# Optimization experiments

Hardware: AMD Instinct MI355X
Metric: run time of the kernel (lower is better)

Reference implementation:

```python
import jax, jax.numpy as jnp
import numpy as np


def setup_inputs() -> dict:
    key = jax.random.key(0)
    ks = jax.random.split(key, 8)
    B, N, H = 8, 64, 256
    nE, E = 256, 64
    HID, OUT = 512, 1
    s1 = 1.0 / np.sqrt(H + E)
    s2 = 1.0 / np.sqrt(HID)
    return {
        "h_all": jax.random.normal(ks[0], (B, N, H), dtype=jnp.float32),
        "e_feat": jax.random.normal(ks[1], (nE, E), dtype=jnp.float32),
        "W1": jax.random.normal(ks[2], (H + E, HID), dtype=jnp.float32) * s1,
        "b1": jnp.zeros((HID,), dtype=jnp.float32),
        "W2": jax.random.normal(ks[3], (HID, HID), dtype=jnp.float32) * s2,
        "b2": jnp.zeros((HID,), dtype=jnp.float32),
        "W3": jax.random.normal(ks[4], (HID, OUT), dtype=jnp.float32) * s2,
        "b3": jnp.zeros((OUT,), dtype=jnp.float32),
    }


def reference(h_all, e_feat, W1, b1, W2, b2, W3, b3):
    # Math == MLP(cat([expand(h), expand(e)], -1)) but computed via split
    # weights: cat([h,e]) @ W1 == h @ W1[:H] + e @ W1[H:], avoiding the
    # materialized [B,N,nE,H+E] concat tensor.
    H = h_all.shape[-1]
    Wh, We = W1[:H], W1[H:]
    h_part = jnp.einsum("bnh,hk->bnk", h_all, Wh)        # [B,N,HID]
    e_part = jnp.einsum("ed,dk->ek", e_feat, We)          # [nE,HID]
    x = h_part[:, :, None, :] + e_part[None, None, :, :] + b1  # [B,N,nE,HID]
    x = jax.nn.relu(x)
    x = jax.nn.relu(jnp.einsum("bnek,kj->bnej", x, W2) + b2)
    return jnp.einsum("bnek,ko->bneo", x, W3) + b3        # [B,N,nE,OUT]
```

## Files before the change

### kernel.cpp

```cpp
#include <hip/hip_runtime.h>
#include <hip/hip_bf16.h>


typedef __attribute__((ext_vector_type(8))) short bf16x8;
typedef __attribute__((ext_vector_type(4))) float f32x4;

static __device__ __forceinline__ ushort2 pk_bf16(float a, float b) {
  union { __hip_bfloat162 h; ushort2 u; } c;
  c.h = __float22bfloat162_rn(make_float2(a, b));
  return c.u;
}
static __device__ __forceinline__ float bf2f(unsigned short u) {
  union { unsigned int i; float f; } c;
  c.i = ((unsigned int)u) << 16;
  return c.f;
}

__global__ __launch_bounds__(256) void k_prep(
    const float* __restrict__ h_all, const float* __restrict__ e_feat,
    const float* __restrict__ W1, const float* __restrict__ b1,
    const float* __restrict__ W2,
    unsigned short* __restrict__ hpb, unsigned short* __restrict__ epb,
    unsigned short* __restrict__ w2f) {
  __shared__ float sm[64 * 68];
  const int t = threadIdx.x;
  const int b = blockIdx.x;

  if (b < 256) {
    const int r0 = b * 2;
    float (*hs)[256] = (float(*)[256])sm;
    hs[0][t] = h_all[(size_t)r0 * 256 + t];
    hs[1][t] = h_all[(size_t)(r0 + 1) * 256 + t];
    __syncthreads();
    float2 a0 = make_float2(0.f, 0.f), a1 = make_float2(0.f, 0.f);
    #pragma unroll 2
    for (int k = 0; k < 256; k += 4) {
      float2 w0 = *(const float2*)(W1 + (size_t)k * 512 + 2 * t);
      float2 w1 = *(const float2*)(W1 + (size_t)(k + 1) * 512 + 2 * t);
      float2 w2v = *(const float2*)(W1 + (size_t)(k + 2) * 512 + 2 * t);
      float2 w3v = *(const float2*)(W1 + (size_t)(k + 3) * 512 + 2 * t);
      float h00 = hs[0][k], h01 = hs[0][k + 1], h02 = hs[0][k + 2], h03 = hs[0][k + 3];
      float h10 = hs[1][k], h11 = hs[1][k + 1], h12 = hs[1][k + 2], h13 = hs[1][k + 3];
      a0.x = fmaf(h00, w0.x, a0.x); a0.y = fmaf(h00, w0.y, a0.y);
      a1.x = fmaf(h10, w0.x, a1.x); a1.y = fmaf(h10, w0.y, a1.y);
      a0.x = fmaf(h01, w1.x, a0.x); a0.y = fmaf(h01, w1.y, a0.y);
      a1.x = fmaf(h11, w1.x, a1.x); a1.y = fmaf(h11, w1.y, a1.y);
      a0.x = fmaf(h02, w2v.x, a0.x); a0.y = fmaf(h02, w2v.y, a0.y);
      a1.x = fmaf(h12, w2v.x, a1.x); a1.y = fmaf(h12, w2v.y, a1.y);
      a0.x = fmaf(h03, w3v.x, a0.x); a0.y = fmaf(h03, w3v.y, a0.y);
      a1.x = fmaf(h13, w3v.x, a1.x); a1.y = fmaf(h13, w3v.y, a1.y);
    }
    float2 bv = *(const float2*)(b1 + 2 * t);
    *(ushort2*)(hpb + (size_t)r0 * 512 + 2 * t) = pk_bf16(a0.x + bv.x, a0.y + bv.y);
    *(ushort2*)(hpb + (size_t)(r0 + 1) * 512 + 2 * t) = pk_bf16(a1.x + bv.x, a1.y + bv.y);
  } else if (b < 288) {
    const int r0 = (b - 256) * 8;
    sm[t] = e_feat[(size_t)r0 * 64 + t];
    sm[256 + t] = e_feat[(size_t)r0 * 64 + 256 + t];
    __syncthreads();
    float2 acc[8];
    #pragma unroll
    for (int i = 0; i < 8; ++i) acc[i] = make_float2(0.f, 0.f);
    for (int k = 0; k < 64; ++k) {
      float2 wv = *(const float2*)(W1 + (size_t)(256 + k) * 512 + 2 * t);
      #pragma unroll
      for (int i = 0; i < 8; ++i) {
        acc[i].x = fmaf(sm[i * 64 + k], wv.x, acc[i].x);
        acc[i].y = fmaf(sm[i * 64 + k], wv.y, acc[i].y);
      }
    }
    #pragma unroll
    for (int i = 0; i < 8; ++i)
      *(ushort2*)(epb + (size_t)(r0 + i) * 512 + 2 * t) = pk_bf16(acc[i].x, acc[i].y);
  } else {
    const int bb = b - 288;
    const int k0 = (bb >> 3) * 64;
    const int c0 = (bb & 7) * 64;
    #pragma unroll
    for (int rr = 0; rr < 4; ++rr) {
      const int row = rr * 16 + (t >> 4);
      float4 v = *(const float4*)(W2 + (size_t)(k0 + row) * 512 + c0 + (t & 15) * 4);
      *(float4*)(&sm[row * 68 + (t & 15) * 4]) = v;
    }
    __syncthreads();
    #pragma unroll
    for (int s2 = 0; s2 < 2; ++s2) {
      const int s = t * 2 + s2;
      const int rec = s >> 6, l = s & 63;
      const int jg = (c0 >> 4) + (rec & 3);
      const int ksg = (k0 >> 5) + (rec >> 2);
      const int cl = (rec & 3) * 16 + (l & 15);
      const int kl = (rec >> 2) * 32 + (l >> 4) * 8;
      union { ushort2 o[4]; uint4 v; } u;
      #pragma unroll
      for (int uu = 0; uu < 4; ++uu)
        u.o[uu] = pk_bf16(sm[(kl + 2 * uu) * 68 + cl], sm[(kl + 2 * uu + 1) * 68 + cl]);
      *(uint4*)(w2f + ((size_t)(jg * 16 + ksg) * 64 + l) * 8) = u.v;
    }
  }
}

__global__ __launch_bounds__(256, 2) void k_main(
    const unsigned short* __restrict__ hpb, const unsigned short* __restrict__ epb,
    const unsigned short* __restrict__ w2f, const float* __restrict__ b2,
    const float* __restrict__ W3, const float* __restrict__ b3,
    float* __restrict__ out) {
  __shared__ unsigned short x1s[64 * 512];

  const int t = threadIdx.x;
  const int lane = t & 63;
  const int w = t >> 6;
  const int l15 = lane & 15, l4 = lane >> 4;
  const int bn = blockIdx.x >> 2;
  const int e0 = (blockIdx.x & 3) << 6;
  const int off = (blockIdx.x * 11) & 15;
  const unsigned short* hprow = hpb + (size_t)bn * 512;

  const unsigned short* wrec = w2f + (size_t)w * 65536 + (size_t)lane * 8;
  bf16x8 bb[2][8];
  #pragma unroll
  for (int j = 0; j < 8; ++j) {
    bb[0][j] = *(const bf16x8*)(wrec + j * 8192 + (size_t)off * 512);
    bb[1][j] = *(const bf16x8*)(wrec + j * 8192 + (size_t)((off + 1) & 15) * 512);
  }

  {
    const int kk = t & 63;
    const int rbase = t >> 6;
    union { uint4 v; unsigned short s[8]; } hv, ev, ov;
    hv.v = *(const uint4*)(hprow + kk * 8);
    float hf[8];
    #pragma unroll
    for (int u = 0; u < 8; ++u) hf[u] = bf2f(hv.s[u]);
    #pragma unroll 2
    for (int rr = 0; rr < 16; ++rr) {
      const int r = rr * 4 + rbase;
      ev.v = *(const uint4*)(epb + (size_t)(e0 + r) * 512 + kk * 8);
      #pragma unroll
      for (int u = 0; u < 4; ++u) {
        ushort2 p = pk_bf16(fmaxf(bf2f(ev.s[2 * u]) + hf[2 * u], 0.f),
                            fmaxf(bf2f(ev.s[2 * u + 1]) + hf[2 * u + 1], 0.f));
        ov.s[2 * u] = p.x;
        ov.s[2 * u + 1] = p.y;
      }
      *(uint4*)(&x1s[r * 512 + (kk ^ (r & 7)) * 8]) = ov.v;
    }
  }
  __syncthreads();

  f32x4 acc[4][8] = {};
  #pragma unroll 4
  for (int ks = 0; ks < 16; ++ks) {
    const int cur = ks & 1;
    const int kr = (ks + off) & 15;
    const int kr2 = (ks + 2 + off) & 15;
    bf16x8 a[4];
    #pragma unroll
    for (int i = 0; i < 4; ++i) {
      const int r = i * 16 + l15;
      a[i] = *(const bf16x8*)(&x1s[r * 512 + (((kr * 4 + l4) ^ (l15 & 7)) * 8)]);
    }
    #pragma unroll
    for (int i = 0; i < 4; ++i)
      #pragma unroll
      for (int j = 0; j < 8; ++j)
        acc[i][j] = __builtin_amdgcn_mfma_f32_16x16x32_bf16(a[i], bb[cur][j], acc[i][j], 0, 0, 0);
    #pragma unroll
    for (int j = 0; j < 8; ++j)
      bb[cur][j] = *(const bf16x8*)(wrec + j * 8192 + (size_t)kr2 * 512);
  }

  float part[16];
  #pragma unroll
  for (int u = 0; u < 16; ++u) part[u] = 0.f;
  #pragma unroll
  for (int j = 0; j < 8; ++j) {
    const int n = w * 128 + j * 16 + l15;
    const float b2v = b2[n], w3v = W3[n];
    #pragma unroll
    for (int i = 0; i < 4; ++i)
      #pragma unroll
      for (int r = 0; r < 4; ++r)
        part[i * 4 + r] = fmaf(fmaxf(acc[i][j][r] + b2v, 0.f), w3v, part[i * 4 + r]);
  }
  #pragma unroll
  for (int u = 0; u < 16; ++u) {
    float v = part[u];
    v += __shfl_xor(v, 1);
    v += __shfl_xor(v, 2);
    v += __shfl_xor(v, 4);
    v += __shfl_xor(v, 8);
    part[u] = v;
  }
  __syncthreads();
  float* osum = (float*)x1s;
  if (l15 == 0) {
    #pragma unroll
    for (int i = 0; i < 4; ++i)
      #pragma unroll
      for (int r = 0; r < 4; ++r)
        osum[w * 64 + i * 16 + l4 * 4 + r] = part[i * 4 + r];
  }
  __syncthreads();
  if (t < 64) {
    float s = b3[0] + osum[t] + osum[64 + t] + osum[128 + t] + osum[192 + t];
    out[(size_t)bn * 256 + e0 + t] = s;
  }
}

extern "C" void kernel_launch(void* const* d_in, const int* in_sizes, int n_in,
                              void* d_out, int out_size, void* d_ws, size_t ws_size,
                              hipStream_t stream) {
  const float* h_all  = (const float*)d_in[0];
  const float* e_feat = (const float*)d_in[1];
  const float* W1     = (const float*)d_in[2];
  const float* b1     = (const float*)d_in[3];
  const float* W2     = (const float*)d_in[4];
  const float* b2     = (const float*)d_in[5];
  const float* W3     = (const float*)d_in[6];
  const float* b3     = (const float*)d_in[7];
  float* out = (float*)d_out;

  unsigned short* hpb = (unsigned short*)d_ws;
  unsigned short* epb = hpb + 512 * 512;
  unsigned short* w2f = epb + 256 * 512;

  hipLaunchKernelGGL(k_prep, dim3(352), dim3(256), 0, stream,
                     h_all, e_feat, W1, b1, W2, hpb, epb, w2f);
  hipLaunchKernelGGL(k_main, dim3(2048), dim3(256), 0, stream,
                     hpb, epb, w2f, b2, W3, b3, out);
}
```

Measured before the change: 145.3 us.

## Switch main GEMM to 32x32x16 MFMA with 512-thread blocks and 8 waves

Replaces the 16x16x32 bf16 MFMA tiling (4 waves each computing 64x128) with 32x32x16 MFMA over 8 waves each computing 64x64. The W2 fragment layout written by the prep kernel is changed to match. Block size goes to 512 threads with launch bounds for higher occupancy, and the epilogue reduction is adapted to 32-lane groups and 8 partial sums. The aim is fewer B-register fragments per wave and better MFMA efficiency. The cost is twice as many waves sharing the LDS tile and a larger epilogue reduction.

```diff
diff --git a/kernel.cpp b/kernel.cpp
--- a/kernel.cpp
+++ b/kernel.cpp
@@ -3,7 +3,7 @@
 
 
 typedef __attribute__((ext_vector_type(8))) short bf16x8;
-typedef __attribute__((ext_vector_type(4))) float f32x4;
+typedef __attribute__((ext_vector_type(16))) float f32x16;
 
 static __device__ __forceinline__ ushort2 pk_bf16(float a, float b) {
   union { __hip_bfloat162 h; ushort2 u; } c;
@@ -73,9 +73,9 @@
     for (int i = 0; i < 8; ++i)
       *(ushort2*)(epb + (size_t)(r0 + i) * 512 + 2 * t) = pk_bf16(acc[i].x, acc[i].y);
   } else {
-    const int bb = b - 288;
-    const int k0 = (bb >> 3) * 64;
-    const int c0 = (bb & 7) * 64;
+    const int bbk = b - 288;
+    const int k0 = (bbk >> 3) * 64;
+    const int c0 = (bbk & 7) * 64;
     #pragma unroll
     for (int rr = 0; rr < 4; ++rr) {
       const int row = rr * 16 + (t >> 4);
@@ -87,20 +87,20 @@
     for (int s2 = 0; s2 < 2; ++s2) {
       const int s = t * 2 + s2;
       const int rec = s >> 6, l = s & 63;
-      const int jg = (c0 >> 4) + (rec & 3);
-      const int ksg = (k0 >> 5) + (rec >> 2);
-      const int cl = (rec & 3) * 16 + (l & 15);
-      const int kl = (rec >> 2) * 32 + (l >> 4) * 8;
+      const int jg = (c0 >> 5) + (rec & 1);
+      const int ks = (k0 >> 4) + (rec >> 1);
+      const int cl = (rec & 1) * 32 + (l & 31);
+      const int kl = (rec >> 1) * 16 + (l >> 5) * 8;
       union { ushort2 o[4]; uint4 v; } u;
       #pragma unroll
       for (int uu = 0; uu < 4; ++uu)
         u.o[uu] = pk_bf16(sm[(kl + 2 * uu) * 68 + cl], sm[(kl + 2 * uu + 1) * 68 + cl]);
-      *(uint4*)(w2f + ((size_t)(jg * 16 + ksg) * 64 + l) * 8) = u.v;
-    }
-  }
-}
-
-__global__ __launch_bounds__(256, 2) void k_main(
+      *(uint4*)(w2f + ((size_t)(jg * 32 + ks) * 64 + l) * 8) = u.v;
+    }
+  }
+}
+
+__global__ __launch_bounds__(512, 4) void k_main(
     const unsigned short* __restrict__ hpb, const unsigned short* __restrict__ epb,
     const unsigned short* __restrict__ w2f, const float* __restrict__ b2,
     const float* __restrict__ W3, const float* __restrict__ b3,
@@ -110,19 +110,19 @@
   const int t = threadIdx.x;
   const int lane = t & 63;
   const int w = t >> 6;
-  const int l15 = lane & 15, l4 = lane >> 4;
+  const int l31 = lane & 31, l5 = lane >> 5;
   const int bn = blockIdx.x >> 2;
   const int e0 = (blockIdx.x & 3) << 6;
-  const int off = (blockIdx.x * 11) & 15;
+  const int off = (blockIdx.x * 7) & 31;
   const unsigned short* hprow = hpb + (size_t)bn * 512;
 
-  const unsigned short* wrec = w2f + (size_t)w * 65536 + (size_t)lane * 8;
-  bf16x8 bb[2][8];
-  #pragma unroll
-  for (int j = 0; j < 8; ++j) {
-    bb[0][j] = *(const bf16x8*)(wrec + j * 8192 + (size_t)off * 512);
-    bb[1][j] = *(const bf16x8*)(wrec + j * 8192 + (size_t)((off + 1) & 15) * 512);
-  }
+  const unsigned short* wrec0 = w2f + (size_t)(w * 2) * 16384 + (size_t)lane * 8;
+  const unsigned short* wrec1 = wrec0 + 16384;
+  bf16x8 bb[2][2];
+  bb[0][0] = *(const bf16x8*)(wrec0 + (size_t)off * 512);
+  bb[0][1] = *(const bf16x8*)(wrec1 + (size_t)off * 512);
+  bb[1][0] = *(const bf16x8*)(wrec0 + (size_t)((off + 1) & 31) * 512);
+  bb[1][1] = *(const bf16x8*)(wrec1 + (size_t)((off + 1) & 31) * 512);
 
   {
     const int kk = t & 63;
@@ -132,9 +132,9 @@
     float hf[8];
     #pragma unroll
     for (int u = 0; u < 8; ++u) hf[u] = bf2f(hv.s[u]);
-    #pragma unroll 2
-    for (int rr = 0; rr < 16; ++rr) {
-      const int r = rr * 4 + rbase;
+    #pragma unroll 4
+    for (int rr = 0; rr < 8; ++rr) {
+      const int r = rr * 8 + rbase;
       ev.v = *(const uint4*)(epb + (size_t)(e0 + r) * 512 + kk * 8);
       #pragma unroll
       for (int u = 0; u < 4; ++u) {
@@ -148,62 +148,65 @@
   }
   __syncthreads();
 
-  f32x4 acc[4][8] = {};
+  const int xr = l31 & 7;
+  f32x16 acc[2][2] = {};
   #pragma unroll 4
-  for (int ks = 0; ks < 16; ++ks) {
+  for (int ks = 0; ks < 32; ++ks) {
     const int cur = ks & 1;
-    const int kr = (ks + off) & 15;
-    const int kr2 = (ks + 2 + off) & 15;
-    bf16x8 a[4];
-    #pragma unroll
-    for (int i = 0; i < 4; ++i) {
-      const int r = i * 16 + l15;
-      a[i] = *(const bf16x8*)(&x1s[r * 512 + (((kr * 4 + l4) ^ (l15 & 7)) * 8)]);
-    }
-    #pragma unroll
-    for (int i = 0; i < 4; ++i)
-      #pragma unroll
-      for (int j = 0; j < 8; ++j)
-        acc[i][j] = __builtin_amdgcn_mfma_f32_16x16x32_bf16(a[i], bb[cur][j], acc[i][j], 0, 0, 0);
-    #pragma unroll
-    for (int j = 0; j < 8; ++j)
-      bb[cur][j] = *(const bf16x8*)(wrec + j * 8192 + (size_t)kr2 * 512);
-  }
-
-  float part[16];
+    const int kr = (ks + off) & 31;
+    const int kr2 = (ks + 2 + off) & 31;
+    const int c0 = ((kr * 2 + l5) ^ xr) * 8;
+    bf16x8 a0 = *(const bf16x8*)(&x1s[l31 * 512 + c0]);
+    bf16x8 a1 = *(const bf16x8*)(&x1s[(l31 + 32) * 512 + c0]);
+    acc[0][0] = __builtin_amdgcn_mfma_f32_32x32x16_bf16(a0, bb[cur][0], acc[0][0], 0, 0, 0);
+    acc[1][0] = __builtin_amdgcn_mfma_f32_32x32x16_bf16(a1, bb[cur][0], acc[1][0], 0, 0, 0);
+    acc[0][1] = __builtin_amdgcn_mfma_f32_32x32x16_bf16(a0, bb[cur][1], acc[0][1], 0, 0, 0);
+    acc[1][1] = __builtin_amdgcn_mfma_f32_32x32x16_bf16(a1, bb[cur][1], acc[1][1], 0, 0, 0);
+    bb[cur][0] = *(const bf16x8*)(wrec0 + (size_t)kr2 * 512);
+    bb[cur][1] = *(const bf16x8*)(wrec1 + (size_t)kr2 * 512);
+  }
+
+  float part[2][16];
   #pragma unroll
-  for (int u = 0; u < 16; ++u) part[u] = 0.f;
+  for (int rt = 0; rt < 2; ++rt)
+    #pragma unroll
+    for (int r = 0; r < 16; ++r) part[rt][r] = 0.f;
   #pragma unroll
-  for (int j = 0; j < 8; ++j) {
-    const int n = w * 128 + j * 16 + l15;
+  for (int ct = 0; ct < 2; ++ct) {
+    const int n = w * 64 + ct * 32 + l31;
     const float b2v = b2[n], w3v = W3[n];
     #pragma unroll
-    for (int i = 0; i < 4; ++i)
-      #pragma unroll
-      for (int r = 0; r < 4; ++r)
-        part[i * 4 + r] = fmaf(fmaxf(acc[i][j][r] + b2v, 0.f), w3v, part[i * 4 + r]);
+    for (int rt = 0; rt < 2; ++rt)
+      #pragma unroll
+      for (int r = 0; r < 16; ++r)
+        part[rt][r] = fmaf(fmaxf(acc[rt][ct][r] + b2v, 0.f), w3v, part[rt][r]);
   }
   #pragma unroll
-  for (int u = 0; u < 16; ++u) {
-    float v = part[u];
-    v += __shfl_xor(v, 1);
-    v += __shfl_xor(v, 2);
-    v += __shfl_xor(v, 4);
-    v += __shfl_xor(v, 8);
-    part[u] = v;
-  }
+  for (int rt = 0; rt < 2; ++rt)
+    #pragma unroll
+    for (int r = 0; r < 16; ++r) {
+      float v = part[rt][r];
+      v += __shfl_xor(v, 1);
+      v += __shfl_xor(v, 2);
+      v += __shfl_xor(v, 4);
+      v += __shfl_xor(v, 8);
+      v += __shfl_xor(v, 16);
+      part[rt][r] = v;
+    }
   __syncthreads();
   float* osum = (float*)x1s;
-  if (l15 == 0) {
-    #pragma unroll
-    for (int i = 0; i < 4; ++i)
-      #pragma unroll
-      for (int r = 0; r < 4; ++r)
-        osum[w * 64 + i * 16 + l4 * 4 + r] = part[i * 4 + r];
+  if (l31 == 0) {
+    #pragma unroll
+    for (int rt = 0; rt < 2; ++rt)
+      #pragma unroll
+      for (int r = 0; r < 16; ++r)
+        osum[w * 64 + rt * 32 + (r & 3) + 8 * (r >> 2) + 4 * l5] = part[rt][r];
   }
   __syncthreads();
   if (t < 64) {
-    float s = b3[0] + osum[t] + osum[64 + t] + osum[128 + t] + osum[192 + t];
+    float s = b3[0];
+    #pragma unroll
+    for (int g = 0; g < 8; ++g) s += osum[g * 64 + t];
     out[(size_t)bn * 256 + e0 + t] = s;
   }
 }
@@ -227,6 +230,6 @@
 
   hipLaunchKernelGGL(k_prep, dim3(352), dim3(256), 0, stream,
                      h_all, e_feat, W1, b1, W2, hpb, epb, w2f);
-  hipLaunchKernelGGL(k_main, dim3(2048), dim3(256), 0, stream,
+  hipLaunchKernelGGL(k_main, dim3(2048), dim3(512), 0, stream,
                      hpb, epb, w2f, b2, W3, b3, out);
 }
```

Result: slower. 164.4 us (+13.1%).

## Store x1 tile in MFMA fragment order and software-pipeline A-fragment LDS loads

Applied to the files above, without the earlier changes.

Builds the relu(h+e) tile in shared memory so each wave writes whole MFMA A-fragments contiguously, indexed by k-step, replacing the XOR-swizzled row layout. This gives conflict-free, lane-contiguous 16-byte LDS reads. The MFMA loop now double-buffers A fragments, prefetching the next k-step's A while issuing the MFMAs, and interleaves the B reloads per column. The build phase now reloads the h vector for every k-chunk instead of keeping it in registers, and the extra af buffer raises register pressure.

```diff
diff --git a/kernel.cpp b/kernel.cpp
--- a/kernel.cpp
+++ b/kernel.cpp
@@ -125,49 +125,46 @@
   }
 
   {
-    const int kk = t & 63;
-    const int rbase = t >> 6;
-    union { uint4 v; unsigned short s[8]; } hv, ev, ov;
-    hv.v = *(const uint4*)(hprow + kk * 8);
-    float hf[8];
-    #pragma unroll
-    for (int u = 0; u < 8; ++u) hf[u] = bf2f(hv.s[u]);
-    #pragma unroll 2
-    for (int rr = 0; rr < 16; ++rr) {
-      const int r = rr * 4 + rbase;
-      ev.v = *(const uint4*)(epb + (size_t)(e0 + r) * 512 + kk * 8);
+    const unsigned short* eprow = epb + (size_t)(e0 + w * 16 + l15) * 512;
+    #pragma unroll 4
+    for (int ksi = 0; ksi < 16; ++ksi) {
+      const int k0 = ksi * 32 + l4 * 8;
+      union { uint4 v; unsigned short s[8]; } hv, ev, ov;
+      hv.v = *(const uint4*)(hprow + k0);
+      ev.v = *(const uint4*)(eprow + k0);
       #pragma unroll
       for (int u = 0; u < 4; ++u) {
-        ushort2 p = pk_bf16(fmaxf(bf2f(ev.s[2 * u]) + hf[2 * u], 0.f),
-                            fmaxf(bf2f(ev.s[2 * u + 1]) + hf[2 * u + 1], 0.f));
+        ushort2 p = pk_bf16(fmaxf(bf2f(hv.s[2 * u]) + bf2f(ev.s[2 * u]), 0.f),
+                            fmaxf(bf2f(hv.s[2 * u + 1]) + bf2f(ev.s[2 * u + 1]), 0.f));
         ov.s[2 * u] = p.x;
         ov.s[2 * u + 1] = p.y;
       }
-      *(uint4*)(&x1s[r * 512 + (kk ^ (r & 7)) * 8]) = ov.v;
+      *(uint4*)(&x1s[(size_t)(w * 16 + ksi) * 512 + lane * 8]) = ov.v;
     }
   }
   __syncthreads();
+
+  bf16x8 af[2][4];
+  #pragma unroll
+  for (int i = 0; i < 4; ++i)
+    af[0][i] = *(const bf16x8*)(&x1s[(size_t)(i * 16 + off) * 512 + lane * 8]);
 
   f32x4 acc[4][8] = {};
   #pragma unroll 4
   for (int ks = 0; ks < 16; ++ks) {
     const int cur = ks & 1;
-    const int kr = (ks + off) & 15;
-    const int kr2 = (ks + 2 + off) & 15;
-    bf16x8 a[4];
-    #pragma unroll
-    for (int i = 0; i < 4; ++i) {
-      const int r = i * 16 + l15;
-      a[i] = *(const bf16x8*)(&x1s[r * 512 + (((kr * 4 + l4) ^ (l15 & 7)) * 8)]);
-    }
-    #pragma unroll
-    for (int i = 0; i < 4; ++i)
-      #pragma unroll
-      for (int j = 0; j < 8; ++j)
-        acc[i][j] = __builtin_amdgcn_mfma_f32_16x16x32_bf16(a[i], bb[cur][j], acc[i][j], 0, 0, 0);
-    #pragma unroll
-    for (int j = 0; j < 8; ++j)
-      bb[cur][j] = *(const bf16x8*)(wrec + j * 8192 + (size_t)kr2 * 512);
+    const int nxt = cur ^ 1;
+    const int kra = (ks + 1 + off) & 15;
+    const int krb = (ks + 2 + off) & 15;
+    #pragma unroll
+    for (int j = 0; j < 8; ++j) {
+      #pragma unroll
+      for (int i = 0; i < 4; ++i)
+        acc[i][j] = __builtin_amdgcn_mfma_f32_16x16x32_bf16(af[cur][i], bb[cur][j], acc[i][j], 0, 0, 0);
+      bb[cur][j] = *(const bf16x8*)(wrec + j * 8192 + (size_t)krb * 512);
+      if (j < 4)
+        af[nxt][j] = *(const bf16x8*)(&x1s[(size_t)(j * 16 + kra) * 512 + lane * 8]);
+    }
   }
 
   float part[16];
```

New measurement: 157.3 us. 1.08x slower.
